# Performance work log

Measured on AMD Instinct MI355X. Metric: run time of the kernel, lower is better.

Reference implementation:

```python
import jax, jax.numpy as jnp
import numpy as np

N_SLOTS = 24   # n_slots from __init__
N_ITERS = 25   # fixed Lloyd iterations (stand-in for sklearn max_iter/convergence)
NORM_EPS = 1e-12  # torch F.normalize eps


def setup_inputs() -> dict:
    key = jax.random.key(0)
    features = jax.random.normal(key, (32, 4096, 256), dtype=jnp.float32)
    return {"features": features}


def _pairwise_sqdist(x, x_sq, centers):
    # x: [B,N,D], x_sq: [B,N,1], centers: [B,K,D] -> [B,N,K]
    c_sq = jnp.sum(centers * centers, axis=-1)  # [B,K]
    return x_sq - 2.0 * jnp.einsum('bnd,bkd->bnk', x, centers) + c_sq[:, None, :]


def _kmeans_batched(x, k, n_iters):
    # x: [B,N,D] -> centers [B,K,D], assignments [B,N]
    B, N, D = x.shape
    # deterministic init: K evenly-spaced points per batch item
    init_idx = jnp.linspace(0, N - 1, k).astype(jnp.int32)
    centers0 = x[:, init_idx, :]  # [B,K,D]
    x_sq = jnp.sum(x * x, axis=-1, keepdims=True)  # [B,N,1]

    def step(centers, _):
        d = _pairwise_sqdist(x, x_sq, centers)          # [B,N,K]
        assign = jnp.argmin(d, axis=-1)                 # [B,N]
        onehot = jax.nn.one_hot(assign, k, dtype=x.dtype)  # [B,N,K]
        counts = jnp.sum(onehot, axis=1)                # [B,K]
        sums = jnp.einsum('bnk,bnd->bkd', onehot, x)    # [B,K,D] scatter-mean numerator
        new_centers = sums / jnp.maximum(counts, 1.0)[..., None]
        # empty clusters keep their previous center
        new_centers = jnp.where(counts[..., None] > 0, new_centers, centers)
        return new_centers, None

    centers, _ = jax.lax.scan(step, centers0, None, length=n_iters)
    final_assign = jnp.argmin(_pairwise_sqdist(x, x_sq, centers), axis=-1)
    return centers, final_assign


def reference(features):
    # L2-normalize along feature dim (use_l2_normalization=True)
    norm = jnp.sqrt(jnp.sum(features * features, axis=-1, keepdims=True))
    f = features / jnp.maximum(norm, NORM_EPS)
    # original detaches before clustering (sklearn on CPU): no gradient flow
    f = jax.lax.stop_gradient(f)
    centers, assign = _kmeans_batched(f, N_SLOTS, N_ITERS)
    # slot masks: one_hot then transpose(-2,-1) -> [B, K, N] float32
    slot_masks = jax.nn.one_hot(assign, N_SLOTS, dtype=jnp.float32).transpose(0, 2, 1)
    return centers, slot_masks
```

## Files before the change

kernel.cpp:

```cpp
#include <hip/hip_runtime.h>
#include <math.h>


#define BATCH 32
#define NPTS 4096
#define DIM 256
#define NSLOT 24
#define NITER 25
#define QPTS 1024

__global__ __launch_bounds__(256) void k_norm(const float* __restrict__ feat,
                                              double* __restrict__ inv_norm) {
  int lane = threadIdx.x & 63;
  int wid = threadIdx.x >> 6;
  int p = blockIdx.x * 4 + wid;
  const float4 v = *(const float4*)(feat + (size_t)p * DIM + lane * 4);
  double s = (double)v.x * v.x + (double)v.y * v.y + (double)v.z * v.z + (double)v.w * v.w;
#pragma unroll
  for (int m = 32; m; m >>= 1) s += __shfl_xor(s, m);
  if (lane == 0) inv_norm[p] = 1.0 / fmax(sqrt(s), 1e-12);
}

__device__ __forceinline__ double block_sum_256(double v, double* red) {
#pragma unroll
  for (int m = 32; m; m >>= 1) v += __shfl_xor(v, m);
  int w = threadIdx.x >> 6;
  if ((threadIdx.x & 63) == 0) red[w] = v;
  __syncthreads();
  return red[0] + red[1] + red[2] + red[3];
}

__global__ __launch_bounds__(256) void k_init_centers(const float* __restrict__ feat,
                                                      const double* __restrict__ inv_norm,
                                                      double* __restrict__ centers,
                                                      float* __restrict__ cT32,
                                                      float* __restrict__ c_sq32) {
  __shared__ double red[4];
  int t = threadIdx.x, k = blockIdx.x, b = blockIdx.y;
  int idx = (int)((double)k * (NPTS - 1) / (NSLOT - 1));
  double v = (double)feat[((size_t)b * NPTS + idx) * DIM + t] * inv_norm[b * NPTS + idx];
  centers[((size_t)b * NSLOT + k) * DIM + t] = v;
  cT32[((size_t)b * DIM + t) * NSLOT + k] = (float)v;
  double s = block_sum_256(v * v, red);
  if (t == 0) c_sq32[b * NSLOT + k] = (float)s;
}

__global__ __launch_bounds__(256) void k_transpose(const float* __restrict__ feat,
                                                   float* __restrict__ xT) {
  __shared__ float tile[64][65];
  int ix = threadIdx.x & 63, iy = threadIdx.x >> 6;
  int bx = blockIdx.x, by = blockIdx.y, b = blockIdx.z;
  const float* fb = feat + ((size_t)b * NPTS + bx * 64) * DIM + by * 64;
#pragma unroll
  for (int r = 0; r < 64; r += 4)
    tile[r + iy][ix] = fb[(size_t)(r + iy) * DIM + ix];
  __syncthreads();
  float* xb = xT + ((size_t)b * DIM + by * 64) * NPTS + bx * 64;
#pragma unroll
  for (int r = 0; r < 64; r += 4)
    xb[(size_t)(r + iy) * NPTS + ix] = tile[ix][r + iy];
}

template <bool USE_T>
__global__ __launch_bounds__(256) void k_assign(const float* __restrict__ feat,
                                                const float* __restrict__ xT,
                                                const double* __restrict__ inv_norm,
                                                const float* __restrict__ cT32,
                                                const float* __restrict__ c_sq32,
                                                int* __restrict__ assign) {
  __shared__ float part[3][64][NSLOT + 1];
  int lane = threadIdx.x & 63;
  int q = __builtin_amdgcn_readfirstlane(threadIdx.x >> 6);
  int blk = blockIdx.x, b = blockIdx.y;
  int n = blk * 64 + lane;
  const float* cb = cT32 + ((size_t)b * DIM + q * 64) * NSLOT;

  float dot[NSLOT];
#pragma unroll
  for (int k = 0; k < NSLOT; ++k) dot[k] = 0.0f;

  for (int d = 0; d < 64; d += 8) {
    float x[8];
    if (USE_T) {
      const float* xp = xT + ((size_t)b * DIM + q * 64 + d) * NPTS + n;
#pragma unroll
      for (int j = 0; j < 8; ++j) x[j] = xp[(size_t)j * NPTS];
    } else {
      float4 v = *(const float4*)(feat + ((size_t)b * NPTS + n) * DIM + q * 64 + d);
      float4 u = *(const float4*)(feat + ((size_t)b * NPTS + n) * DIM + q * 64 + d + 4);
      x[0] = v.x; x[1] = v.y; x[2] = v.z; x[3] = v.w;
      x[4] = u.x; x[5] = u.y; x[6] = u.z; x[7] = u.w;
    }
    const float* cp = cb + (size_t)d * NSLOT;
#pragma unroll
    for (int k = 0; k < NSLOT; ++k) {
      float s = dot[k];
#pragma unroll
      for (int j = 0; j < 8; ++j) s = fmaf(x[j], cp[j * NSLOT + k], s);
      dot[k] = s;
    }
  }

  if (q) {
#pragma unroll
    for (int k = 0; k < NSLOT; ++k) part[q - 1][lane][k] = dot[k];
  }
  __syncthreads();

  if (q == 0) {
    float inv = (float)inv_norm[b * NPTS + n];
    const float* csq = c_sq32 + b * NSLOT;
    int a = 0;
    float best = 0.0f;
#pragma unroll
    for (int k = 0; k < NSLOT; ++k) {
      float df = dot[k] + part[0][lane][k] + part[1][lane][k] + part[2][lane][k];
      float s = csq[k] - 2.0f * (df * inv);
      if (k == 0) { best = s; }
      else if (s < best) { best = s; a = k; }
    }
    assign[b * NPTS + n] = a;
  }
}

__global__ __launch_bounds__(256) void k_cluster4(const float* __restrict__ feat,
                                                  const double* __restrict__ inv_norm,
                                                  const int* __restrict__ assign,
                                                  double* __restrict__ psumG,
                                                  int* __restrict__ cntG) {
  __shared__ unsigned short list[QPTS];
  __shared__ int wtot[4];
  __shared__ double part[4][DIM];

  int id = blockIdx.x;
  int q = id & 3;
  int r = id >> 2;
  int k = r % NSLOT;
  int b = r / NSLOT;

  int t = threadIdx.x;
  int lane = t & 63;
  int w = __builtin_amdgcn_readfirstlane(t >> 6);

  const int* ab = assign + b * NPTS + q * QPTS;
  int base = 0;
  for (int rr = 0; rr < QPTS / 256; ++rr) {
    bool m = (ab[rr * 256 + t] == k);
    unsigned long long bal = __ballot(m);
    int rank = __popcll(bal & ((1ull << lane) - 1ull));
    if (lane == 0) wtot[w] = __popcll(bal);
    __syncthreads();
    int off = base;
#pragma unroll
    for (int w2 = 0; w2 < 3; ++w2)
      if (w2 < w) off += wtot[w2];
    if (m) list[off + rank] = (unsigned short)(rr * 256 + t);
    base += wtot[0] + wtot[1] + wtot[2] + wtot[3];
    __syncthreads();
  }
  int mcount = base;

  const float* fb = feat + ((size_t)b * NPTS + q * QPTS) * DIM + lane * 4;
  const double* ib = inv_norm + b * NPTS + q * QPTS;
  double a0 = 0.0, a1 = 0.0, a2 = 0.0, a3 = 0.0;

  for (int i = w; i < mcount; i += 16) {
    bool h1 = (i + 4) < mcount, h2 = (i + 8) < mcount, h3 = (i + 12) < mcount;
    int n0 = __builtin_amdgcn_readfirstlane((int)list[i]);
    int n1 = __builtin_amdgcn_readfirstlane((int)list[h1 ? i + 4 : i]);
    int n2 = __builtin_amdgcn_readfirstlane((int)list[h2 ? i + 8 : i]);
    int n3 = __builtin_amdgcn_readfirstlane((int)list[h3 ? i + 12 : i]);
    float4 v0 = *(const float4*)(fb + (size_t)n0 * DIM);
    float4 v1 = *(const float4*)(fb + (size_t)n1 * DIM);
    float4 v2 = *(const float4*)(fb + (size_t)n2 * DIM);
    float4 v3 = *(const float4*)(fb + (size_t)n3 * DIM);
    double i0 = ib[n0], i1 = ib[n1], i2 = ib[n2], i3 = ib[n3];
    a0 += (double)v0.x * i0; a1 += (double)v0.y * i0;
    a2 += (double)v0.z * i0; a3 += (double)v0.w * i0;
    if (h1) { a0 += (double)v1.x * i1; a1 += (double)v1.y * i1;
              a2 += (double)v1.z * i1; a3 += (double)v1.w * i1; }
    if (h2) { a0 += (double)v2.x * i2; a1 += (double)v2.y * i2;
              a2 += (double)v2.z * i2; a3 += (double)v2.w * i2; }
    if (h3) { a0 += (double)v3.x * i3; a1 += (double)v3.y * i3;
              a2 += (double)v3.z * i3; a3 += (double)v3.w * i3; }
  }

  part[w][lane * 4 + 0] = a0;
  part[w][lane * 4 + 1] = a1;
  part[w][lane * 4 + 2] = a2;
  part[w][lane * 4 + 3] = a3;
  __syncthreads();

  double s = ((part[0][t] + part[1][t]) + part[2][t]) + part[3][t];
  psumG[(size_t)id * DIM + t] = s;
  if (t == 0) cntG[id] = mcount;
}

__global__ __launch_bounds__(256) void k_upd2(const double* __restrict__ psumG,
                                              const int* __restrict__ cntG,
                                              double* __restrict__ centers,
                                              float* __restrict__ cT32,
                                              float* __restrict__ c_sq32) {
  __shared__ double red[4];
  int t = threadIdx.x, k = blockIdx.x, b = blockIdx.y;
  int id = (b * NSLOT + k) * 4;
  const double* p = psumG + (size_t)id * DIM;
  double s = ((p[t] + p[DIM + t]) + p[2 * DIM + t]) + p[3 * DIM + t];
  int cnt = cntG[id] + cntG[id + 1] + cntG[id + 2] + cntG[id + 3];

  size_t ci = ((size_t)b * NSLOT + k) * DIM + t;
  double nc = (cnt > 0) ? (s / (double)cnt) : centers[ci];
  centers[ci] = nc;
  cT32[((size_t)b * DIM + t) * NSLOT + k] = (float)nc;
  double sq = block_sum_256(nc * nc, red);
  if (t == 0) c_sq32[b * NSLOT + k] = (float)sq;
}

__global__ __launch_bounds__(256) void k_mask(const int* __restrict__ assign,
                                              float* __restrict__ masks) {
  int t = threadIdx.x, nc = blockIdx.x, k = blockIdx.y, b = blockIdx.z;
  int n = nc * 256 + t;
  masks[((size_t)b * NSLOT + k) * NPTS + n] = (assign[b * NPTS + n] == k) ? 1.0f : 0.0f;
}

__global__ __launch_bounds__(256) void k_copyc(const double* __restrict__ centers,
                                               float* __restrict__ out_centers) {
  int t = threadIdx.x, k = blockIdx.x, b = blockIdx.y;
  size_t i = ((size_t)b * NSLOT + k) * DIM + t;
  out_centers[i] = (float)centers[i];
}

extern "C" void kernel_launch(void* const* d_in, const int* in_sizes, int n_in,
                              void* d_out, int out_size, void* d_ws, size_t ws_size,
                              hipStream_t stream) {
  (void)in_sizes; (void)n_in; (void)out_size;
  const float* feat = (const float*)d_in[0];
  float* out_centers = (float*)d_out;
  float* out_masks = out_centers + (size_t)BATCH * NSLOT * DIM;

  char* ws = (char*)d_ws;
  double* inv_norm = (double*)ws; ws += (size_t)BATCH * NPTS * 8;
  double* centers  = (double*)ws; ws += (size_t)BATCH * NSLOT * DIM * 8;
  float* cT32      = (float*)ws;  ws += (size_t)BATCH * DIM * NSLOT * 4;
  float* c_sq32    = (float*)ws;  ws += (size_t)BATCH * NSLOT * 4;
  int* assign      = (int*)ws;    ws += (size_t)BATCH * NPTS * 4;
  double* psumG    = (double*)ws; ws += (size_t)BATCH * NSLOT * 4 * DIM * 8;
  int* cntG        = (int*)ws;    ws += (size_t)BATCH * NSLOT * 4 * 4;
  float* xT        = (float*)ws;
  size_t need_xT = (size_t)(ws - (char*)d_ws) + (size_t)BATCH * DIM * NPTS * 4;
  bool useT = ws_size >= need_xT;

  k_norm<<<BATCH * NPTS / 4, 256, 0, stream>>>(feat, inv_norm);
  k_init_centers<<<dim3(NSLOT, BATCH), 256, 0, stream>>>(feat, inv_norm, centers,
                                                         cT32, c_sq32);
  if (useT)
    k_transpose<<<dim3(NPTS / 64, DIM / 64, BATCH), 256, 0, stream>>>(feat, xT);

  for (int it = 0; it <= NITER; ++it) {
    if (useT)
      k_assign<true><<<dim3(NPTS / 64, BATCH), 256, 0, stream>>>(feat, xT, inv_norm,
                                                                 cT32, c_sq32, assign);
    else
      k_assign<false><<<dim3(NPTS / 64, BATCH), 256, 0, stream>>>(feat, xT, inv_norm,
                                                                  cT32, c_sq32, assign);
    if (it == NITER) break;
    k_cluster4<<<NSLOT * BATCH * 4, 256, 0, stream>>>(feat, inv_norm, assign,
                                                      psumG, cntG);
    k_upd2<<<dim3(NSLOT, BATCH), 256, 0, stream>>>(psumG, cntG, centers, cT32, c_sq32);
  }

  k_mask<<<dim3(NPTS / 256, NSLOT, BATCH), 256, 0, stream>>>(assign, out_masks);
  k_copyc<<<dim3(NSLOT, BATCH), 256, 0, stream>>>(centers, out_centers);
}
```

Before: 1.730 ms.

## Split batch into two groups for cache residency and fuse mask write into final assign

```diff
diff --git a/kernel.cpp b/kernel.cpp
--- a/kernel.cpp
+++ b/kernel.cpp
@@ -3,6 +3,8 @@
 
 
 #define BATCH 32
+#define GB 16
+#define NGROUP 2
 #define NPTS 4096
 #define DIM 256
 #define NSLOT 24
@@ -61,17 +63,19 @@
     xb[(size_t)(r + iy) * NPTS + ix] = tile[ix][r + iy];
 }
 
-template <bool USE_T>
+template <bool USE_T, bool FINAL>
 __global__ __launch_bounds__(256) void k_assign(const float* __restrict__ feat,
                                                 const float* __restrict__ xT,
                                                 const double* __restrict__ inv_norm,
                                                 const float* __restrict__ cT32,
                                                 const float* __restrict__ c_sq32,
-                                                int* __restrict__ assign) {
+                                                int* __restrict__ assign,
+                                                float* __restrict__ masks,
+                                                int b0) {
   __shared__ float part[3][64][NSLOT + 1];
   int lane = threadIdx.x & 63;
   int q = __builtin_amdgcn_readfirstlane(threadIdx.x >> 6);
-  int blk = blockIdx.x, b = blockIdx.y;
+  int blk = blockIdx.x, b = blockIdx.y + b0;
   int n = blk * 64 + lane;
   const float* cb = cT32 + ((size_t)b * DIM + q * 64) * NSLOT;
 
@@ -119,7 +123,13 @@
       if (k == 0) { best = s; }
       else if (s < best) { best = s; a = k; }
     }
-    assign[b * NPTS + n] = a;
+    if (FINAL) {
+#pragma unroll
+      for (int k = 0; k < NSLOT; ++k)
+        masks[((size_t)b * NSLOT + k) * NPTS + n] = (a == k) ? 1.0f : 0.0f;
+    } else {
+      assign[b * NPTS + n] = a;
+    }
   }
 }
 
@@ -127,7 +137,8 @@
                                                   const double* __restrict__ inv_norm,
                                                   const int* __restrict__ assign,
                                                   double* __restrict__ psumG,
-                                                  int* __restrict__ cntG) {
+                                                  int* __restrict__ cntG,
+                                                  int b0) {
   __shared__ unsigned short list[QPTS];
   __shared__ int wtot[4];
   __shared__ double part[4][DIM];
@@ -136,7 +147,8 @@
   int q = id & 3;
   int r = id >> 2;
   int k = r % NSLOT;
-  int b = r / NSLOT;
+  int b = r / NSLOT + b0;
+  int gid = ((b * NSLOT) + k) * 4 + q;
 
   int t = threadIdx.x;
   int lane = t & 63;
@@ -192,17 +204,18 @@
   __syncthreads();
 
   double s = ((part[0][t] + part[1][t]) + part[2][t]) + part[3][t];
-  psumG[(size_t)id * DIM + t] = s;
-  if (t == 0) cntG[id] = mcount;
+  psumG[(size_t)gid * DIM + t] = s;
+  if (t == 0) cntG[gid] = mcount;
 }
 
 __global__ __launch_bounds__(256) void k_upd2(const double* __restrict__ psumG,
                                               const int* __restrict__ cntG,
                                               double* __restrict__ centers,
                                               float* __restrict__ cT32,
-                                              float* __restrict__ c_sq32) {
+                                              float* __restrict__ c_sq32,
+                                              int b0) {
   __shared__ double red[4];
-  int t = threadIdx.x, k = blockIdx.x, b = blockIdx.y;
+  int t = threadIdx.x, k = blockIdx.x, b = blockIdx.y + b0;
   int id = (b * NSLOT + k) * 4;
   const double* p = psumG + (size_t)id * DIM;
   double s = ((p[t] + p[DIM + t]) + p[2 * DIM + t]) + p[3 * DIM + t];
@@ -214,13 +227,6 @@
   cT32[((size_t)b * DIM + t) * NSLOT + k] = (float)nc;
   double sq = block_sum_256(nc * nc, red);
   if (t == 0) c_sq32[b * NSLOT + k] = (float)sq;
-}
-
-__global__ __launch_bounds__(256) void k_mask(const int* __restrict__ assign,
-                                              float* __restrict__ masks) {
-  int t = threadIdx.x, nc = blockIdx.x, k = blockIdx.y, b = blockIdx.z;
-  int n = nc * 256 + t;
-  masks[((size_t)b * NSLOT + k) * NPTS + n] = (assign[b * NPTS + n] == k) ? 1.0f : 0.0f;
 }
 
 __global__ __launch_bounds__(256) void k_copyc(const double* __restrict__ centers,
@@ -238,16 +244,16 @@
   float* out_centers = (float*)d_out;
   float* out_masks = out_centers + (size_t)BATCH * NSLOT * DIM;
 
-  char* ws = (char*)d_ws;
-  double* inv_norm = (double*)ws; ws += (size_t)BATCH * NPTS * 8;
-  double* centers  = (double*)ws; ws += (size_t)BATCH * NSLOT * DIM * 8;
-  float* cT32      = (float*)ws;  ws += (size_t)BATCH * DIM * NSLOT * 4;
-  float* c_sq32    = (float*)ws;  ws += (size_t)BATCH * NSLOT * 4;
-  int* assign      = (int*)ws;    ws += (size_t)BATCH * NPTS * 4;
-  double* psumG    = (double*)ws; ws += (size_t)BATCH * NSLOT * 4 * DIM * 8;
-  int* cntG        = (int*)ws;    ws += (size_t)BATCH * NSLOT * 4 * 4;
-  float* xT        = (float*)ws;
-  size_t need_xT = (size_t)(ws - (char*)d_ws) + (size_t)BATCH * DIM * NPTS * 4;
+  char* p = (char*)d_ws;
+  double* inv_norm = (double*)p; p += (size_t)BATCH * NPTS * 8;
+  double* centers  = (double*)p; p += (size_t)BATCH * NSLOT * DIM * 8;
+  float* cT32      = (float*)p;  p += (size_t)BATCH * DIM * NSLOT * 4;
+  float* c_sq32    = (float*)p;  p += (size_t)BATCH * NSLOT * 4;
+  int* assign      = (int*)p;    p += (size_t)BATCH * NPTS * 4;
+  double* psumG    = (double*)p; p += (size_t)BATCH * NSLOT * 4 * DIM * 8;
+  int* cntG        = (int*)p;    p += (size_t)BATCH * NSLOT * 4 * 4;
+  float* xT        = (float*)p;
+  size_t need_xT = (size_t)(p - (char*)d_ws) + (size_t)BATCH * DIM * NPTS * 4;
   bool useT = ws_size >= need_xT;
 
   k_norm<<<BATCH * NPTS / 4, 256, 0, stream>>>(feat, inv_norm);
@@ -256,19 +262,33 @@
   if (useT)
     k_transpose<<<dim3(NPTS / 64, DIM / 64, BATCH), 256, 0, stream>>>(feat, xT);
 
-  for (int it = 0; it <= NITER; ++it) {
-    if (useT)
-      k_assign<true><<<dim3(NPTS / 64, BATCH), 256, 0, stream>>>(feat, xT, inv_norm,
-                                                                 cT32, c_sq32, assign);
-    else
-      k_assign<false><<<dim3(NPTS / 64, BATCH), 256, 0, stream>>>(feat, xT, inv_norm,
-                                                                  cT32, c_sq32, assign);
-    if (it == NITER) break;
-    k_cluster4<<<NSLOT * BATCH * 4, 256, 0, stream>>>(feat, inv_norm, assign,
-                                                      psumG, cntG);
-    k_upd2<<<dim3(NSLOT, BATCH), 256, 0, stream>>>(psumG, cntG, centers, cT32, c_sq32);
-  }
-
-  k_mask<<<dim3(NPTS / 256, NSLOT, BATCH), 256, 0, stream>>>(assign, out_masks);
+  for (int g = 0; g < NGROUP; ++g) {
+    int b0 = g * GB;
+    for (int it = 0; it <= NITER; ++it) {
+      bool fin = (it == NITER);
+      dim3 ag(NPTS / 64, GB);
+      if (useT) {
+        if (fin)
+          k_assign<true, true><<<ag, 256, 0, stream>>>(feat, xT, inv_norm, cT32,
+                                                       c_sq32, assign, out_masks, b0);
+        else
+          k_assign<true, false><<<ag, 256, 0, stream>>>(feat, xT, inv_norm, cT32,
+                                                        c_sq32, assign, out_masks, b0);
+      } else {
+        if (fin)
+          k_assign<false, true><<<ag, 256, 0, stream>>>(feat, xT, inv_norm, cT32,
+                                                        c_sq32, assign, out_masks, b0);
+        else
+          k_assign<false, false><<<ag, 256, 0, stream>>>(feat, xT, inv_norm, cT32,
+                                                         c_sq32, assign, out_masks, b0);
+      }
+      if (fin) break;
+      k_cluster4<<<NSLOT * GB * 4, 256, 0, stream>>>(feat, inv_norm, assign,
+                                                     psumG, cntG, b0);
+      k_upd2<<<dim3(NSLOT, GB), 256, 0, stream>>>(psumG, cntG, centers,
+                                                  cT32, c_sq32, b0);
+    }
+  }
+
   k_copyc<<<dim3(NSLOT, BATCH), 256, 0, stream>>>(centers, out_centers);
 }
```

After: 1.829 ms. 1.06x slower.
